# Kernel optimization log

Hardware: AMD Instinct MI355X
Metric: run time of the kernel (lower is better)

Reference implementation:

```python
import jax, jax.numpy as jnp
import numpy as np

N_NODES = 100000
N_EDGES = 50000
NNZ = 800000
C = 256
EPS = 0.0  # fixed (train_eps=False)


def setup_inputs() -> dict:
    key = jax.random.key(0)
    k1, k2, k3, k4, k5 = jax.random.split(key, 5)
    x_0 = jax.random.normal(k1, (N_NODES, C), dtype=jnp.float32)
    node_idx = jax.random.randint(k2, (NNZ,), 0, N_NODES, dtype=jnp.int64 if jax.config.jax_enable_x64 else jnp.int32)
    edge_idx = jax.random.randint(k3, (NNZ,), 0, N_EDGES, dtype=jnp.int64 if jax.config.jax_enable_x64 else jnp.int32)
    W = jax.random.normal(k4, (C, C), dtype=jnp.float32) / np.sqrt(C)
    b = jax.random.normal(k5, (C,), dtype=jnp.float32) * 0.01
    return {"x_0": x_0, "node_idx": node_idx, "edge_idx": edge_idx, "W": W, "b": b}


def reference(x_0, node_idx, edge_idx, W, b):
    # vertex2edge: x_1 = B_1^T @ x_0  (each hyperedge sums its member nodes)
    x_1 = jax.ops.segment_sum(x_0[node_idx], edge_idx, num_segments=N_EDGES)  # (E, C)
    # edge2vertex: m_{1->0} = B_1 @ x_1  (each node sums its incident hyperedges)
    m_1_0 = jax.ops.segment_sum(x_1[edge_idx], node_idx, num_segments=N_NODES)  # (N, C)
    # GIN update: Theta @ ((1+eps) x_0 + m)
    x_0_out = ((1.0 + EPS) * x_0 + m_1_0) @ W.T + b
    # use_norm=False -> no row normalization
    return (x_0_out, x_1)
```

## Files before the change

### kernel.cpp

```cpp
#include <hip/hip_runtime.h>

#define N_NODES 100000
#define N_EDGES 50000
#define NNZ     800000
#define C       256

#define SHC_E 8
#define SHC_N 9
#define NBC_E ((N_EDGES + (1 << SHC_E) - 1) >> SHC_E)
#define NBC_N ((N_NODES + (1 << SHC_N) - 1) >> SHC_N)
#define CHUNK 4096
#define NCHUNK ((NNZ + CHUNK - 1) / CHUNK)

#define NBLK_E ((N_EDGES + 1023) / 1024)
#define NBLK_N ((N_NODES + 1023) / 1024)
#define CONV_BLOCKS (N_NODES * C / 4 / 256)
#define HIST_BLOCKS (NNZ / 256)

typedef short  bf16x8 __attribute__((ext_vector_type(8)));
typedef float  f32x4  __attribute__((ext_vector_type(4)));

static __device__ __forceinline__ unsigned short f2bf(float f) {
    unsigned int u = __float_as_uint(f);
    u += 0x7FFF + ((u >> 16) & 1);
    return (unsigned short)(u >> 16);
}
static __device__ __forceinline__ float bf2f(unsigned short u) {
    return __uint_as_float(((unsigned int)u) << 16);
}


__global__ void convert_hist(const float* __restrict__ x0, unsigned short* __restrict__ x0b,
                             const int* __restrict__ node_idx, const int* __restrict__ edge_idx,
                             int* __restrict__ cnt_n, int* __restrict__ cnt_e) {
    int bid = blockIdx.x;
    if (bid < CONV_BLOCKS) {
        size_t i = (size_t)bid * 256 + threadIdx.x;
        float4 v = ((const float4*)x0)[i];
        ushort4 o;
        o.x = f2bf(v.x); o.y = f2bf(v.y); o.z = f2bf(v.z); o.w = f2bf(v.w);
        ((ushort4*)x0b)[i] = o;
    } else {
        int j = (bid - CONV_BLOCKS) * 256 + threadIdx.x;
        atomicAdd(&cnt_n[node_idx[j]], 1);
        atomicAdd(&cnt_e[edge_idx[j]], 1);
    }
}


__global__ void prep_w(const float* __restrict__ W, unsigned short* __restrict__ Wb) {
    int idx = blockIdx.x * 256 + threadIdx.x;
    int h = idx >> 12, i = idx & 4095;
    int t = i >> 9, s = (i >> 6) & 7, l = i & 63;
    int m = l & 15, q = l >> 4;
    const float* src = W + (size_t)(h * 128 + 16 * t + m) * C + 32 * s + 8 * q;
    float4 f0 = *(const float4*)(src);
    float4 f1 = *(const float4*)(src + 4);
    unsigned short* d = Wb + (size_t)idx * 8;
    d[0] = f2bf(f0.x); d[1] = f2bf(f0.y); d[2] = f2bf(f0.z); d[3] = f2bf(f0.w);
    d[4] = f2bf(f1.x); d[5] = f2bf(f1.y); d[6] = f2bf(f1.z); d[7] = f2bf(f1.w);
}


__global__ void scan_partials2(const int* __restrict__ cnt_e, const int* __restrict__ cnt_n,
                               int* __restrict__ part_e, int* __restrict__ part_n) {
    bool isE = blockIdx.x < NBLK_E;
    const int* cnt = isE ? cnt_e : cnt_n;
    int* partials = isE ? part_e : part_n;
    int n = isE ? N_EDGES : N_NODES;
    int bid = isE ? blockIdx.x : blockIdx.x - NBLK_E;
    int tid = threadIdx.x, lane = tid & 63, wid = tid >> 6;
    int base = bid * 1024 + tid * 4;
    int s = 0;
    if (base < n) { int4 v = *(const int4*)(cnt + base); s = v.x + v.y + v.z + v.w; }
#pragma unroll
    for (int o = 1; o < 64; o <<= 1) s += __shfl_down(s, o, 64);
    __shared__ int ws[4];
    if (lane == 0) ws[wid] = s;
    __syncthreads();
    if (tid == 0) partials[bid] = ws[0] + ws[1] + ws[2] + ws[3];
}

__global__ void scan_small2(int* __restrict__ part_e, int* __restrict__ part_n,
                            int* __restrict__ off_e_last, int* __restrict__ off_n_last) {
    int* partials = (blockIdx.x == 0) ? part_e : part_n;
    int nb = (blockIdx.x == 0) ? NBLK_E : NBLK_N;
    int* off_last = (blockIdx.x == 0) ? off_e_last : off_n_last;
    int tid = threadIdx.x, lane = tid & 63, wid = tid >> 6;
    int v = (tid < nb) ? partials[tid] : 0;
    int incl = v;
#pragma unroll
    for (int s = 1; s < 64; s <<= 1) { int u = __shfl_up(incl, s, 64); if (lane >= s) incl += u; }
    __shared__ int wsum[2];
    if (lane == 63) wsum[wid] = incl;
    __syncthreads();
    int excl = incl - v + (wid == 1 ? wsum[0] : 0);
    if (tid < nb) partials[tid] = excl;
    if (tid == 0) *off_last = NNZ;
}

__global__ void scan_final2(const int* __restrict__ cnt_e, const int* __restrict__ cnt_n,
                            const int* __restrict__ part_e, const int* __restrict__ part_n,
                            int* __restrict__ off_e, int* __restrict__ off_n,
                            int* __restrict__ gcur_e, int* __restrict__ gcur_n) {
    bool isE = blockIdx.x < NBLK_E;
    const int* cnt = isE ? cnt_e : cnt_n;
    const int* partials = isE ? part_e : part_n;
    int* off = isE ? off_e : off_n;
    int* gcur = isE ? gcur_e : gcur_n;
    int shc = isE ? SHC_E : SHC_N;
    int n = isE ? N_EDGES : N_NODES;
    int bid = isE ? blockIdx.x : blockIdx.x - NBLK_E;
    int tid = threadIdx.x, lane = tid & 63, wid = tid >> 6;
    int base = bid * 1024 + tid * 4;
    int v0 = 0, v1 = 0, v2 = 0, v3 = 0;
    if (base < n) { int4 v = *(const int4*)(cnt + base); v0 = v.x; v1 = v.y; v2 = v.z; v3 = v.w; }
    int tsum = v0 + v1 + v2 + v3;
    int incl = tsum;
#pragma unroll
    for (int s = 1; s < 64; s <<= 1) { int u = __shfl_up(incl, s, 64); if (lane >= s) incl += u; }
    __shared__ int ws[4], wexcl[4];
    if (lane == 63) ws[wid] = incl;
    __syncthreads();
    if (tid == 0) { int c = 0; for (int i = 0; i < 4; i++) { wexcl[i] = c; c += ws[i]; } }
    __syncthreads();
    if (base < n) {
        int b = partials[bid] + wexcl[wid] + (incl - tsum);
        off[base]     = b;
        off[base + 1] = b + v0;
        off[base + 2] = b + v0 + v1;
        off[base + 3] = b + v0 + v1 + v2;
        if ((base & ((1 << shc) - 1)) == 0) gcur[base >> shc] = b;
    }
}


__global__ __launch_bounds__(256) void bin_coarse(const int* __restrict__ node_idx,
                                                  const int* __restrict__ edge_idx,
                                                  int* __restrict__ gcur_e, int* __restrict__ gcur_n,
                                                  unsigned int* __restrict__ tmp_e,
                                                  unsigned int* __restrict__ tmp_n) {
    __shared__ int hist_e[NBC_E], hist_n[NBC_N];
    __shared__ int base_e[NBC_E], base_n[NBC_N];
    const int tid = threadIdx.x;
    const int start = blockIdx.x * CHUNK;
    const int end = (start + CHUNK < NNZ) ? start + CHUNK : NNZ;

    for (int i = tid; i < NBC_E; i += 256) hist_e[i] = 0;
    for (int i = tid; i < NBC_N; i += 256) hist_n[i] = 0;
    __syncthreads();

    for (int k = start + tid; k < end; k += 256) {
        atomicAdd(&hist_e[edge_idx[k] >> SHC_E], 1);
        atomicAdd(&hist_n[node_idx[k] >> SHC_N], 1);
    }
    __syncthreads();

    for (int i = tid; i < NBC_E; i += 256) {
        int c = hist_e[i];
        base_e[i] = c ? atomicAdd(&gcur_e[i], c) : 0;
        hist_e[i] = 0;
    }
    for (int i = tid; i < NBC_N; i += 256) {
        int c = hist_n[i];
        base_n[i] = c ? atomicAdd(&gcur_n[i], c) : 0;
        hist_n[i] = 0;
    }
    __syncthreads();

    for (int k = start + tid; k < end; k += 256) {
        int ni = node_idx[k], ei = edge_idx[k];
        int be = ei >> SHC_E;
        int pe = base_e[be] + atomicAdd(&hist_e[be], 1);
        tmp_e[pe] = ((unsigned int)ni << SHC_E) | (unsigned int)(ei & ((1 << SHC_E) - 1));
        int bn = ni >> SHC_N;
        int pn = base_n[bn] + atomicAdd(&hist_n[bn], 1);
        tmp_n[pn] = ((unsigned int)ei << SHC_N) | (unsigned int)(ni & ((1 << SHC_N) - 1));
    }
}

__global__ __launch_bounds__(256) void scatter_fine(const unsigned int* __restrict__ tmp_e,
                                                    const unsigned int* __restrict__ tmp_n,
                                                    const int* __restrict__ off_e,
                                                    const int* __restrict__ off_n,
                                                    int* __restrict__ perm_e,
                                                    int* __restrict__ perm_n) {
    __shared__ int cur[1 << SHC_N];
    bool isE = blockIdx.x < NBC_E;
    const unsigned int* tmp = isE ? tmp_e : tmp_n;
    const int* off = isE ? off_e : off_n;
    int* perm = isE ? perm_e : perm_n;
    int b = isE ? blockIdx.x : blockIdx.x - NBC_E;
    int shc = isE ? SHC_E : SHC_N;
    int n = isE ? N_EDGES : N_NODES;
    const int tid = threadIdx.x;
    const int kbase = b << shc;
    const int nk = 1 << shc;
    for (int t = tid; t < nk; t += 256) {
        int key = kbase + t;
        cur[t] = off[key < n ? key : n];
    }
    const int start = off[kbase];
    int endk = kbase + nk;
    const int end = off[endk < n ? endk : n];
    __syncthreads();
    for (int k = start + tid; k < end; k += 256) {
        unsigned int u = tmp[k];
        int pos = atomicAdd(&cur[u & (nk - 1)], 1);
        perm[pos] = (int)(u >> shc);
    }
}


__global__ void pull_edge(const unsigned short* __restrict__ x0b,
                          const int* __restrict__ off, const int* __restrict__ perm,
                          float* __restrict__ x1, unsigned short* __restrict__ x1b) {
    int e = blockIdx.x * 4 + (threadIdx.x >> 6);
    int lane = threadIdx.x & 63;
    int s0 = off[e], s1 = off[e + 1];
    float a0 = 0, a1 = 0, a2 = 0, a3 = 0;
    float b0 = 0, b1 = 0, b2 = 0, b3 = 0;
    float c0 = 0, c1 = 0, c2 = 0, c3 = 0;
    float d0 = 0, d1 = 0, d2 = 0, d3 = 0;
    int k = s0;
    for (; k + 4 <= s1; k += 4) {
        int r0 = perm[k], r1 = perm[k + 1], r2 = perm[k + 2], r3 = perm[k + 3];
        ushort4 u0 = *(const ushort4*)(x0b + (size_t)r0 * C + lane * 4);
        ushort4 u1 = *(const ushort4*)(x0b + (size_t)r1 * C + lane * 4);
        ushort4 u2 = *(const ushort4*)(x0b + (size_t)r2 * C + lane * 4);
        ushort4 u3 = *(const ushort4*)(x0b + (size_t)r3 * C + lane * 4);
        a0 += bf2f(u0.x); a1 += bf2f(u0.y); a2 += bf2f(u0.z); a3 += bf2f(u0.w);
        b0 += bf2f(u1.x); b1 += bf2f(u1.y); b2 += bf2f(u1.z); b3 += bf2f(u1.w);
        c0 += bf2f(u2.x); c1 += bf2f(u2.y); c2 += bf2f(u2.z); c3 += bf2f(u2.w);
        d0 += bf2f(u3.x); d1 += bf2f(u3.y); d2 += bf2f(u3.z); d3 += bf2f(u3.w);
    }
    for (; k < s1; k++) {
        int r0 = perm[k];
        ushort4 u0 = *(const ushort4*)(x0b + (size_t)r0 * C + lane * 4);
        a0 += bf2f(u0.x); a1 += bf2f(u0.y); a2 += bf2f(u0.z); a3 += bf2f(u0.w);
    }
    a0 += b0 + c0 + d0; a1 += b1 + c1 + d1; a2 += b2 + c2 + d2; a3 += b3 + c3 + d3;
    f32x4 v = {a0, a1, a2, a3};
    __builtin_nontemporal_store(v, (f32x4*)(x1 + (size_t)e * C + lane * 4));
    ushort4 o; o.x = f2bf(a0); o.y = f2bf(a1); o.z = f2bf(a2); o.w = f2bf(a3);
    *(ushort4*)(x1b + (size_t)e * C + lane * 4) = o;
}

__global__ void pull_node(const float* __restrict__ x0, const unsigned short* __restrict__ x1b,
                          const int* __restrict__ off, const int* __restrict__ perm,
                          unsigned short* __restrict__ xm) {
    int n = blockIdx.x * 4 + (threadIdx.x >> 6);
    int lane = threadIdx.x & 63;
    int s0 = off[n], s1 = off[n + 1];
    const float4 x = *(const float4*)(x0 + (size_t)n * C + lane * 4);
    float a0 = x.x, a1 = x.y, a2 = x.z, a3 = x.w;
    float b0 = 0, b1 = 0, b2 = 0, b3 = 0;
    float c0 = 0, c1 = 0, c2 = 0, c3 = 0;
    float d0 = 0, d1 = 0, d2 = 0, d3 = 0;
    int k = s0;
    for (; k + 4 <= s1; k += 4) {
        int r0 = perm[k], r1 = perm[k + 1], r2 = perm[k + 2], r3 = perm[k + 3];
        ushort4 u0 = *(const ushort4*)(x1b + (size_t)r0 * C + lane * 4);
        ushort4 u1 = *(const ushort4*)(x1b + (size_t)r1 * C + lane * 4);
        ushort4 u2 = *(const ushort4*)(x1b + (size_t)r2 * C + lane * 4);
        ushort4 u3 = *(const ushort4*)(x1b + (size_t)r3 * C + lane * 4);
        a0 += bf2f(u0.x); a1 += bf2f(u0.y); a2 += bf2f(u0.z); a3 += bf2f(u0.w);
        b0 += bf2f(u1.x); b1 += bf2f(u1.y); b2 += bf2f(u1.z); b3 += bf2f(u1.w);
        c0 += bf2f(u2.x); c1 += bf2f(u2.y); c2 += bf2f(u2.z); c3 += bf2f(u2.w);
        d0 += bf2f(u3.x); d1 += bf2f(u3.y); d2 += bf2f(u3.z); d3 += bf2f(u3.w);
    }
    for (; k < s1; k++) {
        int r0 = perm[k];
        ushort4 u0 = *(const ushort4*)(x1b + (size_t)r0 * C + lane * 4);
        a0 += bf2f(u0.x); a1 += bf2f(u0.y); a2 += bf2f(u0.z); a3 += bf2f(u0.w);
    }
    a0 += b0 + c0 + d0; a1 += b1 + c1 + d1; a2 += b2 + c2 + d2; a3 += b3 + c3 + d3;
    ushort4 o; o.x = f2bf(a0); o.y = f2bf(a1); o.z = f2bf(a2); o.w = f2bf(a3);
    *(ushort4*)(xm + (size_t)n * C + lane * 4) = o;
}

__global__ __launch_bounds__(512) void mfma_gemm2(const unsigned short* __restrict__ xm,
                                                  const unsigned short* __restrict__ Wb,
                                                  const float* __restrict__ bias,
                                                  float* __restrict__ out) {
    __shared__ unsigned short Bs[8 * 8 * 64 * 8];
    const int rt = blockIdx.x >> 1;
    const int colbase = (blockIdx.x & 1) * 128;
    const int tid = threadIdx.x;

    const unsigned short* wsrc = Wb + (size_t)(blockIdx.x & 1) * (4096 * 8);
#pragma unroll
    for (int it = 0; it < 8; it++) {
        int i = it * 512 + tid;
        *(bf16x8*)(Bs + (size_t)i * 8) = *(const bf16x8*)(wsrc + (size_t)i * 8);
    }

    const int w = tid >> 6, lane = tid & 63;
    const int m = lane & 15, q = lane >> 4;
    const int row = rt * 128 + w * 16 + m;
    const int arow = row < N_NODES ? row : N_NODES - 1;

    bf16x8 a[8];
    const unsigned short* ap = xm + (size_t)arow * C + q * 8;
#pragma unroll
    for (int s = 0; s < 8; s++) a[s] = *(const bf16x8*)(ap + 32 * s);

    __syncthreads();

    f32x4 acc[8];
#pragma unroll
    for (int t = 0; t < 8; t++) acc[t] = (f32x4){0.f, 0.f, 0.f, 0.f};

#pragma unroll
    for (int s = 0; s < 8; s++) {
#pragma unroll
        for (int t = 0; t < 8; t++) {
            bf16x8 b = *(const bf16x8*)(Bs + ((t * 8 + s) * 64 + lane) * 8);
            acc[t] = __builtin_amdgcn_mfma_f32_16x16x32_bf16(a[s], b, acc[t], 0, 0, 0);
        }
    }

    const int r0 = rt * 128 + w * 16 + q * 4;
#pragma unroll
    for (int t = 0; t < 8; t++) {
        float bv = bias[colbase + t * 16 + m];
#pragma unroll
        for (int r = 0; r < 4; r++) {
            int rr = r0 + r;
            if (rr < N_NODES)
                out[(size_t)rr * C + colbase + t * 16 + m] = acc[t][r] + bv;
        }
    }
}


__global__ void init_kernel(const float* __restrict__ x0, float* __restrict__ out) {
    long long i = (long long)blockIdx.x * blockDim.x + threadIdx.x;
    const long long n_node4 = (long long)N_NODES * C / 4;
    const long long n_tot4  = (long long)(N_NODES + N_EDGES) * C / 4;
    float4* o4 = (float4*)out;
    if (i < n_node4)      o4[i] = ((const float4*)x0)[i];
    else if (i < n_tot4)  o4[i] = make_float4(0.f, 0.f, 0.f, 0.f);
}

__global__ void scatter_add_kernel(const float* __restrict__ src,
                                   const int* __restrict__ src_idx,
                                   const int* __restrict__ dst_idx,
                                   float* __restrict__ dst) {
    int j    = blockIdx.x * (blockDim.x >> 6) + (threadIdx.x >> 6);
    int lane = threadIdx.x & 63;
    if (j >= NNZ) return;
    int s = src_idx[j];
    int d = dst_idx[j];
    const float4 v = *(const float4*)(src + (long long)s * C + lane * 4);
    float* dp = dst + (long long)d * C + lane * 4;
    atomicAdd(dp + 0, v.x); atomicAdd(dp + 1, v.y);
    atomicAdd(dp + 2, v.z); atomicAdd(dp + 3, v.w);
}

__global__ void gin_gemm_kernel(const float* __restrict__ W,
                                const float* __restrict__ b,
                                float* __restrict__ out) {
    int n = blockIdx.x;
    int t = threadIdx.x;
    __shared__ float xs[C];
    float* row = out + (long long)n * C;
    xs[t] = row[t];
    __syncthreads();
    float acc = b[t];
    const float* wrow = W + t * C;
#pragma unroll 8
    for (int k = 0; k < C; k += 4) {
        float4 xv = *(const float4*)(xs + k);
        float4 wv = *(const float4*)(wrow + k);
        acc = fmaf(xv.x, wv.x, acc); acc = fmaf(xv.y, wv.y, acc);
        acc = fmaf(xv.z, wv.z, acc); acc = fmaf(xv.w, wv.w, acc);
    }
    row[t] = acc;
}


extern "C" void kernel_launch(void* const* d_in, const int* in_sizes, int n_in,
                              void* d_out, int out_size, void* d_ws, size_t ws_size,
                              hipStream_t stream) {
    const float* x0       = (const float*)d_in[0];
    const int*   node_idx = (const int*)d_in[1];
    const int*   edge_idx = (const int*)d_in[2];
    const float* W        = (const float*)d_in[3];
    const float* b        = (const float*)d_in[4];
    float* out = (float*)d_out;
    float* x1  = out + (size_t)N_NODES * C;

    char* p = (char*)d_ws;
    size_t used = 0;
    auto alloc = [&](size_t bytes) {
        char* r = p + used;
        used += (bytes + 255) & ~(size_t)255;
        return r;
    };
    int* off_e  = (int*)alloc((N_EDGES + 1) * 4);
    int* off_n  = (int*)alloc((N_NODES + 1) * 4);
    int* cnt_e  = (int*)alloc(N_EDGES * 4);
    int* cnt_n  = (int*)alloc(N_NODES * 4);
    int* part_e = (int*)alloc(128 * 4);
    int* part_n = (int*)alloc(128 * 4);
    int* gcur_e = (int*)alloc(NBC_E * 4);
    int* gcur_n = (int*)alloc(NBC_N * 4);
    int* perm_e = (int*)alloc((size_t)NNZ * 4);
    int* perm_n = (int*)alloc((size_t)NNZ * 4);
    unsigned short* Wb  = (unsigned short*)alloc((size_t)2 * 4096 * 8 * 2);
    unsigned short* x0b = (unsigned short*)alloc((size_t)N_NODES * C * 2);
    unsigned short* x1b = (unsigned short*)alloc((size_t)N_EDGES * C * 2);
    unsigned short* xm  = (unsigned short*)alloc((size_t)N_NODES * C * 2);

    if (ws_size < used) {
        long long tot4 = (long long)(N_NODES + N_EDGES) * C / 4;
        init_kernel<<<(int)((tot4 + 255) / 256), 256, 0, stream>>>(x0, out);
        int grid = NNZ / 4;
        scatter_add_kernel<<<grid, 256, 0, stream>>>(x0, node_idx, edge_idx, x1);
        scatter_add_kernel<<<grid, 256, 0, stream>>>(x1, edge_idx, node_idx, out);
        gin_gemm_kernel<<<N_NODES, 256, 0, stream>>>(W, b, out);
        return;
    }

    hipMemsetAsync(cnt_e, 0, (size_t)((char*)cnt_n - (char*)cnt_e) + (size_t)N_NODES * 4, stream);

    convert_hist<<<CONV_BLOCKS + HIST_BLOCKS, 256, 0, stream>>>(x0, x0b, node_idx, edge_idx, cnt_n, cnt_e);

    prep_w<<<32, 256, 0, stream>>>(W, Wb);

    scan_partials2<<<NBLK_E + NBLK_N, 256, 0, stream>>>(cnt_e, cnt_n, part_e, part_n);
    scan_small2<<<2, 128, 0, stream>>>(part_e, part_n, off_e + N_EDGES, off_n + N_NODES);
    scan_final2<<<NBLK_E + NBLK_N, 256, 0, stream>>>(cnt_e, cnt_n, part_e, part_n,
                                                     off_e, off_n, gcur_e, gcur_n);

    unsigned int* tmp_e = (unsigned int*)x1b;
    unsigned int* tmp_n = (unsigned int*)xm;
    bin_coarse<<<NCHUNK, 256, 0, stream>>>(node_idx, edge_idx, gcur_e, gcur_n, tmp_e, tmp_n);
    scatter_fine<<<NBC_E + NBC_N, 256, 0, stream>>>(tmp_e, tmp_n, off_e, off_n, perm_e, perm_n);

    pull_edge<<<N_EDGES / 4, 256, 0, stream>>>(x0b, off_e, perm_e, x1, x1b);
    pull_node<<<N_NODES / 4, 256, 0, stream>>>(x0, x1b, off_n, perm_n, xm);

    const int row_tiles = (N_NODES + 127) / 128;
    mfma_gemm2<<<row_tiles * 2, 512, 0, stream>>>(xm, Wb, b, out);
}
```

Before: 499.7 us.

## Replace fine-grained count histogram and three-pass scan with coarse-bucket counts

Measured after the change: 452.6 us. -9.4%, faster.

```diff
diff --git a/kernel.cpp b/kernel.cpp
--- a/kernel.cpp
+++ b/kernel.cpp
@@ -12,10 +12,7 @@
 #define CHUNK 4096
 #define NCHUNK ((NNZ + CHUNK - 1) / CHUNK)
 
-#define NBLK_E ((N_EDGES + 1023) / 1024)
-#define NBLK_N ((N_NODES + 1023) / 1024)
 #define CONV_BLOCKS (N_NODES * C / 4 / 256)
-#define HIST_BLOCKS (NNZ / 256)
 
 typedef short  bf16x8 __attribute__((ext_vector_type(8)));
 typedef float  f32x4  __attribute__((ext_vector_type(4)));
@@ -32,7 +29,7 @@
 
 __global__ void convert_hist(const float* __restrict__ x0, unsigned short* __restrict__ x0b,
                              const int* __restrict__ node_idx, const int* __restrict__ edge_idx,
-                             int* __restrict__ cnt_n, int* __restrict__ cnt_e) {
+                             int* __restrict__ gcnt_e, int* __restrict__ gcnt_n) {
     int bid = blockIdx.x;
     if (bid < CONV_BLOCKS) {
         size_t i = (size_t)bid * 256 + threadIdx.x;
@@ -41,9 +38,20 @@
         o.x = f2bf(v.x); o.y = f2bf(v.y); o.z = f2bf(v.z); o.w = f2bf(v.w);
         ((ushort4*)x0b)[i] = o;
     } else {
-        int j = (bid - CONV_BLOCKS) * 256 + threadIdx.x;
-        atomicAdd(&cnt_n[node_idx[j]], 1);
-        atomicAdd(&cnt_e[edge_idx[j]], 1);
+        __shared__ int he[NBC_E], hn[NBC_N];
+        const int tid = threadIdx.x;
+        for (int i = tid; i < NBC_E; i += 256) he[i] = 0;
+        for (int i = tid; i < NBC_N; i += 256) hn[i] = 0;
+        __syncthreads();
+        const int start = (bid - CONV_BLOCKS) * CHUNK;
+        const int end = (start + CHUNK < NNZ) ? start + CHUNK : NNZ;
+        for (int k = start + tid; k < end; k += 256) {
+            atomicAdd(&he[edge_idx[k] >> SHC_E], 1);
+            atomicAdd(&hn[node_idx[k] >> SHC_N], 1);
+        }
+        __syncthreads();
+        for (int i = tid; i < NBC_E; i += 256) if (he[i]) atomicAdd(&gcnt_e[i], he[i]);
+        for (int i = tid; i < NBC_N; i += 256) if (hn[i]) atomicAdd(&gcnt_n[i], hn[i]);
     }
 }
 
@@ -62,76 +70,26 @@
 }
 
 
-__global__ void scan_partials2(const int* __restrict__ cnt_e, const int* __restrict__ cnt_n,
-                               int* __restrict__ part_e, int* __restrict__ part_n) {
-    bool isE = blockIdx.x < NBLK_E;
-    const int* cnt = isE ? cnt_e : cnt_n;
-    int* partials = isE ? part_e : part_n;
-    int n = isE ? N_EDGES : N_NODES;
-    int bid = isE ? blockIdx.x : blockIdx.x - NBLK_E;
+__global__ void coarse_scan(const int* __restrict__ gcnt_e, const int* __restrict__ gcnt_n,
+                            int* __restrict__ gbase_e, int* __restrict__ gbase_n,
+                            int* __restrict__ gcur_e, int* __restrict__ gcur_n) {
+    const int* gcnt = (blockIdx.x == 0) ? gcnt_e : gcnt_n;
+    int* gbase = (blockIdx.x == 0) ? gbase_e : gbase_n;
+    int* gcur  = (blockIdx.x == 0) ? gcur_e : gcur_n;
+    const int nb = (blockIdx.x == 0) ? NBC_E : NBC_N;
     int tid = threadIdx.x, lane = tid & 63, wid = tid >> 6;
-    int base = bid * 1024 + tid * 4;
-    int s = 0;
-    if (base < n) { int4 v = *(const int4*)(cnt + base); s = v.x + v.y + v.z + v.w; }
-#pragma unroll
-    for (int o = 1; o < 64; o <<= 1) s += __shfl_down(s, o, 64);
-    __shared__ int ws[4];
-    if (lane == 0) ws[wid] = s;
-    __syncthreads();
-    if (tid == 0) partials[bid] = ws[0] + ws[1] + ws[2] + ws[3];
-}
-
-__global__ void scan_small2(int* __restrict__ part_e, int* __restrict__ part_n,
-                            int* __restrict__ off_e_last, int* __restrict__ off_n_last) {
-    int* partials = (blockIdx.x == 0) ? part_e : part_n;
-    int nb = (blockIdx.x == 0) ? NBLK_E : NBLK_N;
-    int* off_last = (blockIdx.x == 0) ? off_e_last : off_n_last;
-    int tid = threadIdx.x, lane = tid & 63, wid = tid >> 6;
-    int v = (tid < nb) ? partials[tid] : 0;
+    int v = (tid < nb) ? gcnt[tid] : 0;
     int incl = v;
 #pragma unroll
     for (int s = 1; s < 64; s <<= 1) { int u = __shfl_up(incl, s, 64); if (lane >= s) incl += u; }
-    __shared__ int wsum[2];
+    __shared__ int wsum[4];
     if (lane == 63) wsum[wid] = incl;
     __syncthreads();
-    int excl = incl - v + (wid == 1 ? wsum[0] : 0);
-    if (tid < nb) partials[tid] = excl;
-    if (tid == 0) *off_last = NNZ;
-}
-
-__global__ void scan_final2(const int* __restrict__ cnt_e, const int* __restrict__ cnt_n,
-                            const int* __restrict__ part_e, const int* __restrict__ part_n,
-                            int* __restrict__ off_e, int* __restrict__ off_n,
-                            int* __restrict__ gcur_e, int* __restrict__ gcur_n) {
-    bool isE = blockIdx.x < NBLK_E;
-    const int* cnt = isE ? cnt_e : cnt_n;
-    const int* partials = isE ? part_e : part_n;
-    int* off = isE ? off_e : off_n;
-    int* gcur = isE ? gcur_e : gcur_n;
-    int shc = isE ? SHC_E : SHC_N;
-    int n = isE ? N_EDGES : N_NODES;
-    int bid = isE ? blockIdx.x : blockIdx.x - NBLK_E;
-    int tid = threadIdx.x, lane = tid & 63, wid = tid >> 6;
-    int base = bid * 1024 + tid * 4;
-    int v0 = 0, v1 = 0, v2 = 0, v3 = 0;
-    if (base < n) { int4 v = *(const int4*)(cnt + base); v0 = v.x; v1 = v.y; v2 = v.z; v3 = v.w; }
-    int tsum = v0 + v1 + v2 + v3;
-    int incl = tsum;
-#pragma unroll
-    for (int s = 1; s < 64; s <<= 1) { int u = __shfl_up(incl, s, 64); if (lane >= s) incl += u; }
-    __shared__ int ws[4], wexcl[4];
-    if (lane == 63) ws[wid] = incl;
-    __syncthreads();
-    if (tid == 0) { int c = 0; for (int i = 0; i < 4; i++) { wexcl[i] = c; c += ws[i]; } }
-    __syncthreads();
-    if (base < n) {
-        int b = partials[bid] + wexcl[wid] + (incl - tsum);
-        off[base]     = b;
-        off[base + 1] = b + v0;
-        off[base + 2] = b + v0 + v1;
-        off[base + 3] = b + v0 + v1 + v2;
-        if ((base & ((1 << shc) - 1)) == 0) gcur[base >> shc] = b;
-    }
+    int add = 0;
+    for (int i = 0; i < wid; i++) add += wsum[i];
+    int excl = add + incl - v;
+    if (tid <= nb) gbase[tid] = excl;
+    if (tid < nb)  gcur[tid]  = excl;
 }
 
 
@@ -179,36 +137,64 @@
     }
 }
 
+
+template <int SHC, int NTOT>
+static __device__ __forceinline__ void scatter_fine_body(const unsigned int* __restrict__ tmp,
+                                                         const int* __restrict__ gbase,
+                                                         int* __restrict__ off,
+                                                         int* __restrict__ perm,
+                                                         int b, int* hist, int* cur, int* wsum) {
+    constexpr int NK = 1 << SHC;
+    const int tid = threadIdx.x, lane = tid & 63, wid = tid >> 6;
+    const int start = gbase[b], end = gbase[b + 1];
+    for (int t = tid; t < NK; t += 256) hist[t] = 0;
+    __syncthreads();
+    for (int k = start + tid; k < end; k += 256)
+        atomicAdd(&hist[tmp[k] & (NK - 1)], 1);
+    __syncthreads();
+    int v0, v1 = 0, local;
+    if constexpr (NK == 512) { v0 = hist[2 * tid]; v1 = hist[2 * tid + 1]; local = v0 + v1; }
+    else                     { v0 = hist[tid]; local = v0; }
+    int incl = local;
+#pragma unroll
+    for (int s = 1; s < 64; s <<= 1) { int u = __shfl_up(incl, s, 64); if (lane >= s) incl += u; }
+    if (lane == 63) wsum[wid] = incl;
+    __syncthreads();
+    int add = 0;
+    for (int i = 0; i < wid; i++) add += wsum[i];
+    int base = start + add + incl - local;
+    const int kbase = b << SHC;
+    if constexpr (NK == 512) {
+        int key0 = kbase + 2 * tid;
+        if (key0 < NTOT)     off[key0] = base;
+        if (key0 + 1 < NTOT) off[key0 + 1] = base + v0;
+        cur[2 * tid]     = base;
+        cur[2 * tid + 1] = base + v0;
+    } else {
+        int key0 = kbase + tid;
+        if (key0 < NTOT) off[key0] = base;
+        cur[tid] = base;
+    }
+    if (b == ((NTOT - 1) >> SHC) && tid == 0) off[NTOT] = end;
+    __syncthreads();
+    for (int k = start + tid; k < end; k += 256) {
+        unsigned int u = tmp[k];
+        int pos = atomicAdd(&cur[u & (NK - 1)], 1);
+        perm[pos] = (int)(u >> SHC);
+    }
+}
+
 __global__ __launch_bounds__(256) void scatter_fine(const unsigned int* __restrict__ tmp_e,
                                                     const unsigned int* __restrict__ tmp_n,
-                                                    const int* __restrict__ off_e,
-                                                    const int* __restrict__ off_n,
-                                                    int* __restrict__ perm_e,
-                                                    int* __restrict__ perm_n) {
-    __shared__ int cur[1 << SHC_N];
-    bool isE = blockIdx.x < NBC_E;
-    const unsigned int* tmp = isE ? tmp_e : tmp_n;
-    const int* off = isE ? off_e : off_n;
-    int* perm = isE ? perm_e : perm_n;
-    int b = isE ? blockIdx.x : blockIdx.x - NBC_E;
-    int shc = isE ? SHC_E : SHC_N;
-    int n = isE ? N_EDGES : N_NODES;
-    const int tid = threadIdx.x;
-    const int kbase = b << shc;
-    const int nk = 1 << shc;
-    for (int t = tid; t < nk; t += 256) {
-        int key = kbase + t;
-        cur[t] = off[key < n ? key : n];
-    }
-    const int start = off[kbase];
-    int endk = kbase + nk;
-    const int end = off[endk < n ? endk : n];
-    __syncthreads();
-    for (int k = start + tid; k < end; k += 256) {
-        unsigned int u = tmp[k];
-        int pos = atomicAdd(&cur[u & (nk - 1)], 1);
-        perm[pos] = (int)(u >> shc);
-    }
+                                                    const int* __restrict__ gbase_e,
+                                                    const int* __restrict__ gbase_n,
+                                                    int* __restrict__ off_e, int* __restrict__ off_n,
+                                                    int* __restrict__ perm_e, int* __restrict__ perm_n) {
+    __shared__ int hist[1 << SHC_N], cur[1 << SHC_N], wsum[4];
+    if (blockIdx.x < NBC_E)
+        scatter_fine_body<SHC_E, N_EDGES>(tmp_e, gbase_e, off_e, perm_e, blockIdx.x, hist, cur, wsum);
+    else
+        scatter_fine_body<SHC_N, N_NODES>(tmp_n, gbase_n, off_n, perm_n, blockIdx.x - NBC_E, hist, cur, wsum);
 }
 
 
@@ -279,6 +265,7 @@
     *(ushort4*)(xm + (size_t)n * C + lane * 4) = o;
 }
 
+
 __global__ __launch_bounds__(512) void mfma_gemm2(const unsigned short* __restrict__ xm,
                                                   const unsigned short* __restrict__ Wb,
                                                   const float* __restrict__ bias,
@@ -398,16 +385,16 @@
         used += (bytes + 255) & ~(size_t)255;
         return r;
     };
-    int* off_e  = (int*)alloc((N_EDGES + 1) * 4);
-    int* off_n  = (int*)alloc((N_NODES + 1) * 4);
-    int* cnt_e  = (int*)alloc(N_EDGES * 4);
-    int* cnt_n  = (int*)alloc(N_NODES * 4);
-    int* part_e = (int*)alloc(128 * 4);
-    int* part_n = (int*)alloc(128 * 4);
-    int* gcur_e = (int*)alloc(NBC_E * 4);
-    int* gcur_n = (int*)alloc(NBC_N * 4);
-    int* perm_e = (int*)alloc((size_t)NNZ * 4);
-    int* perm_n = (int*)alloc((size_t)NNZ * 4);
+    int* off_e   = (int*)alloc((N_EDGES + 1) * 4);
+    int* off_n   = (int*)alloc((N_NODES + 1) * 4);
+    int* gcnt_e  = (int*)alloc(NBC_E * 4);
+    int* gcnt_n  = (int*)alloc(NBC_N * 4);
+    int* gbase_e = (int*)alloc((NBC_E + 1) * 4);
+    int* gbase_n = (int*)alloc((NBC_N + 1) * 4);
+    int* gcur_e  = (int*)alloc(NBC_E * 4);
+    int* gcur_n  = (int*)alloc(NBC_N * 4);
+    int* perm_e  = (int*)alloc((size_t)NNZ * 4);
+    int* perm_n  = (int*)alloc((size_t)NNZ * 4);
     unsigned short* Wb  = (unsigned short*)alloc((size_t)2 * 4096 * 8 * 2);
     unsigned short* x0b = (unsigned short*)alloc((size_t)N_NODES * C * 2);
     unsigned short* x1b = (unsigned short*)alloc((size_t)N_EDGES * C * 2);
@@ -423,21 +410,20 @@
         return;
     }
 
-    hipMemsetAsync(cnt_e, 0, (size_t)((char*)cnt_n - (char*)cnt_e) + (size_t)N_NODES * 4, stream);
-
-    convert_hist<<<CONV_BLOCKS + HIST_BLOCKS, 256, 0, stream>>>(x0, x0b, node_idx, edge_idx, cnt_n, cnt_e);
+    hipMemsetAsync(gcnt_e, 0, (size_t)((char*)gcnt_n - (char*)gcnt_e) + (size_t)NBC_N * 4, stream);
+
+    convert_hist<<<CONV_BLOCKS + NCHUNK, 256, 0, stream>>>(x0, x0b, node_idx, edge_idx,
+                                                           gcnt_e, gcnt_n);
 
     prep_w<<<32, 256, 0, stream>>>(W, Wb);
 
-    scan_partials2<<<NBLK_E + NBLK_N, 256, 0, stream>>>(cnt_e, cnt_n, part_e, part_n);
-    scan_small2<<<2, 128, 0, stream>>>(part_e, part_n, off_e + N_EDGES, off_n + N_NODES);
-    scan_final2<<<NBLK_E + NBLK_N, 256, 0, stream>>>(cnt_e, cnt_n, part_e, part_n,
-                                                     off_e, off_n, gcur_e, gcur_n);
+    coarse_scan<<<2, 256, 0, stream>>>(gcnt_e, gcnt_n, gbase_e, gbase_n, gcur_e, gcur_n);
 
     unsigned int* tmp_e = (unsigned int*)x1b;
     unsigned int* tmp_n = (unsigned int*)xm;
     bin_coarse<<<NCHUNK, 256, 0, stream>>>(node_idx, edge_idx, gcur_e, gcur_n, tmp_e, tmp_n);
-    scatter_fine<<<NBC_E + NBC_N, 256, 0, stream>>>(tmp_e, tmp_n, off_e, off_n, perm_e, perm_n);
+    scatter_fine<<<NBC_E + NBC_N, 256, 0, stream>>>(tmp_e, tmp_n, gbase_e, gbase_n,
+                                                    off_e, off_n, perm_e, perm_n);
 
     pull_edge<<<N_EDGES / 4, 256, 0, stream>>>(x0b, off_e, perm_e, x1, x1b);
     pull_node<<<N_NODES / 4, 256, 0, stream>>>(x0, x1b, off_n, perm_n, xm);
```
